# Kernel optimization log

Hardware: AMD Instinct MI355X
Metric: run time of the kernel (lower is better)

Reference implementation:

```python
import jax, jax.numpy as jnp
import numpy as np

B, T, C = 4, 8192, 1024
H, D = 16, 64  # n_head, head_dim


def setup_inputs() -> dict:
    key = jax.random.key(0)
    ks = jax.random.split(key, 9)
    s = 1.0 / np.sqrt(C)
    return {
        "x": jax.random.normal(ks[0], (B, T, C), jnp.float32),
        "Wq": jax.random.uniform(ks[1], (C, C), jnp.float32, -s, s),
        "bq": jax.random.uniform(ks[2], (C,), jnp.float32, -s, s),
        "Wk": jax.random.uniform(ks[3], (C, C), jnp.float32, -s, s),
        "bk": jax.random.uniform(ks[4], (C,), jnp.float32, -s, s),
        "Wv": jax.random.uniform(ks[5], (C, C), jnp.float32, -s, s),
        "bv": jax.random.uniform(ks[6], (C,), jnp.float32, -s, s),
        "Wp": jax.random.uniform(ks[7], (C, C), jnp.float32, -s, s),
        "bp": jax.random.uniform(ks[8], (C,), jnp.float32, -s, s),
    }


def _heads(t):
    # (B,T,C) -> (B,H,T,D)
    return t.reshape(B, T, H, D).transpose(0, 2, 1, 3)


def reference(x, Wq, bq, Wk, bk, Wv, bv, Wp, bp):
    q = _heads(x @ Wq.T + bq)
    k = _heads(x @ Wk.T + bk)
    v = _heads(x @ Wv.T + bv)
    # attn_type='l1': softmax q,k over feature dim; L1 normalizer
    q = jax.nn.softmax(q, axis=-1)
    k = jax.nn.softmax(k, axis=-1)
    k_sum = k.sum(axis=-2, keepdims=True)               # (B,H,1,D)
    D_inv = 1.0 / (q * k_sum).sum(axis=-1, keepdims=True)  # (B,H,T,1)
    context = jnp.einsum('bhtd,bhte->bhde', k, v)       # (B,H,D,D)
    out = jnp.einsum('bhtd,bhde->bhte', q, context) * D_inv + q
    out = out.transpose(0, 2, 1, 3).reshape(B, T, C)
    return out @ Wp.T + bp
```

## Files before the change

kernel.cpp:

```cpp
#include <hip/hip_runtime.h>
#include <hip/hip_bf16.h>
#include <stdint.h>


#define BT    32768
#define CDIM  1024

using bf16 = __hip_bfloat16;
typedef short  short8   __attribute__((ext_vector_type(8)));
typedef short  short4_t __attribute__((ext_vector_type(4)));
typedef unsigned short ushort4_t __attribute__((ext_vector_type(4)));
typedef float  floatx4  __attribute__((ext_vector_type(4)));

__device__ __forceinline__ float bfbits2f(unsigned short u) {
    union { unsigned int i; float f; } c; c.i = ((unsigned int)u) << 16; return c.f;
}

__device__ __forceinline__ void gld_lds16(const void* g, void* lds) {
    __builtin_amdgcn_global_load_lds(
        (const __attribute__((address_space(1))) uint32_t*)g,
        (__attribute__((address_space(3))) uint32_t*)lds,
        16, 0, 0);
}

__global__ void zero_kernel(float* __restrict__ p) {
    p[(size_t)blockIdx.x * 256 + threadIdx.x] = 0.0f;
}

__global__ void cvt_kernel(const float* __restrict__ x,
                           const float* __restrict__ Wq, const float* __restrict__ Wk,
                           const float* __restrict__ Wv, const float* __restrict__ Wp,
                           bf16* __restrict__ xb, bf16* __restrict__ Wb) {
    const int XF4 = (BT * CDIM) / 4;
    int i = blockIdx.x * 256 + threadIdx.x;
    const float* src; bf16* dst; int off;
    if (i < XF4) { src = x; dst = xb; off = i; }
    else {
        int i2 = i - XF4;
        int wi = i2 >> 18;
        off = i2 & 0x3FFFF;
        src = (wi == 0) ? Wq : (wi == 1) ? Wk : (wi == 2) ? Wv : Wp;
        dst = Wb + (size_t)wi * 1048576;
    }
    float4 f = ((const float4*)src)[off];
    union { bf16 h[4]; short4_t v; } u;
    u.h[0] = __float2bfloat16(f.x); u.h[1] = __float2bfloat16(f.y);
    u.h[2] = __float2bfloat16(f.z); u.h[3] = __float2bfloat16(f.w);
    *(short4_t*)(dst + (size_t)off * 4) = u.v;
}

__global__ __launch_bounds__(256)
void gemm_qkv(const bf16* __restrict__ A, const bf16* __restrict__ Bw,
              const float* __restrict__ bq, const float* __restrict__ bk,
              const float* __restrict__ bv,
              bf16* __restrict__ qb, bf16* __restrict__ kb, bf16* __restrict__ vb) {
    __shared__ bf16 sA[128 * 32];
    __shared__ bf16 sB[128 * 32];
    int tid = threadIdx.x, lane = tid & 63, wv = tid >> 6;
    int bn = blockIdx.x % 24;
    int bm = blockIdx.x / 24;
    const bf16* Ab = A  + (size_t)bm * 128 * CDIM;
    const bf16* Bb = Bw + (size_t)bn * 128 * CDIM;
    int srow = lane >> 2;
    int scol = ((lane & 3) ^ ((lane >> 3) & 3)) * 8;

    floatx4 acc[4][4] = {};
    int quad = lane >> 4, l15 = lane & 15;
    int m0 = (wv & 1) * 64, n0v = (wv >> 1) * 64;
    int rpos = (quad ^ ((l15 >> 1) & 3)) * 8;

    for (int kt = 0; kt < 32; ++kt) {
        int k0 = kt * 32;
        #pragma unroll
        for (int c = 0; c < 2; ++c) {
            int chunk = wv * 2 + c;
            gld_lds16(Ab + (size_t)(chunk * 16 + srow) * CDIM + k0 + scol, &sA[chunk * 512]);
            gld_lds16(Bb + (size_t)(chunk * 16 + srow) * CDIM + k0 + scol, &sB[chunk * 512]);
        }
        __syncthreads();
        short8 af[4], bfr[4];
        #pragma unroll
        for (int i = 0; i < 4; ++i) {
            af[i]  = *(const short8*)&sA[(m0  + i * 16 + l15) * 32 + rpos];
            bfr[i] = *(const short8*)&sB[(n0v + i * 16 + l15) * 32 + rpos];
        }
        #pragma unroll
        for (int i = 0; i < 4; ++i)
            #pragma unroll
            for (int j = 0; j < 4; ++j)
                acc[i][j] = __builtin_amdgcn_mfma_f32_16x16x32_bf16(af[i], bfr[j], acc[i][j], 0, 0, 0);
        __syncthreads();
    }

    int grow0 = bm * 128 + m0;
    int n_abs = bn * 128 + n0v;
    bf16* dst; const float* biasp; int ncol0; bool smax;
    if (n_abs < 1024)      { dst = qb; biasp = bq; ncol0 = n_abs;        smax = true;  }
    else if (n_abs < 2048) { dst = kb; biasp = bk; ncol0 = n_abs - 1024; smax = true;  }
    else                   { dst = vb; biasp = bv; ncol0 = n_abs - 2048; smax = false; }
    float bias4[4];
    #pragma unroll
    for (int j = 0; j < 4; ++j) bias4[j] = biasp[ncol0 + j * 16 + l15];

    #pragma unroll
    for (int i = 0; i < 4; ++i) {
        #pragma unroll
        for (int r = 0; r < 4; ++r) {
            float vals[4];
            #pragma unroll
            for (int j = 0; j < 4; ++j) vals[j] = acc[i][j][r] + bias4[j];
            if (smax) {
                float mx = fmaxf(fmaxf(vals[0], vals[1]), fmaxf(vals[2], vals[3]));
                #pragma unroll
                for (int d = 1; d < 16; d <<= 1) mx = fmaxf(mx, __shfl_xor(mx, d));
                float s = 0.f;
                #pragma unroll
                for (int j = 0; j < 4; ++j) { vals[j] = __expf(vals[j] - mx); s += vals[j]; }
                #pragma unroll
                for (int d = 1; d < 16; d <<= 1) s += __shfl_xor(s, d);
                float rinv = 1.0f / s;
                #pragma unroll
                for (int j = 0; j < 4; ++j) vals[j] *= rinv;
            }
            size_t row = (size_t)(grow0 + i * 16 + quad * 4 + r);
            #pragma unroll
            for (int j = 0; j < 4; ++j)
                dst[row * 1024 + ncol0 + j * 16 + l15] = __float2bfloat16(vals[j]);
        }
    }
}

__global__ __launch_bounds__(256)
void ctx_kernel(const bf16* __restrict__ kbuf, const bf16* __restrict__ vbuf,
                float* __restrict__ ctx, float* __restrict__ ksum) {
    int bid = blockIdx.x;
    int head = bid >> 4, chunk = bid & 15;
    int b = head >> 4, h = head & 15;
    size_t rowbase = (size_t)b * 8192 + (size_t)chunk * 512;
    int coff = h * 64;
    __shared__ bf16 ks[64 * 64];
    __shared__ bf16 vs[64 * 64];
    int tid = threadIdx.x;
    int lrow = tid >> 2, lpart = tid & 3;
    int di = tid >> 4, ei = tid & 15;

    float acc[16];
    #pragma unroll
    for (int i = 0; i < 16; ++i) acc[i] = 0.f;
    float ksv[4] = {0.f, 0.f, 0.f, 0.f};

    size_t gbase = (rowbase + lrow) * 1024 + coff + lpart * 16;
    short8 pk0 = *(const short8*)(kbuf + gbase);
    short8 pk1 = *(const short8*)(kbuf + gbase + 8);
    short8 pv0 = *(const short8*)(vbuf + gbase);
    short8 pv1 = *(const short8*)(vbuf + gbase + 8);

    for (int st = 0; st < 8; ++st) {
        __syncthreads();
        *(short8*)&ks[lrow * 64 + lpart * 16]     = pk0;
        *(short8*)&ks[lrow * 64 + lpart * 16 + 8] = pk1;
        *(short8*)&vs[lrow * 64 + lpart * 16]     = pv0;
        *(short8*)&vs[lrow * 64 + lpart * 16 + 8] = pv1;
        __syncthreads();
        if (st < 7) {
            size_t g = gbase + (size_t)(st + 1) * 64 * 1024;
            pk0 = *(const short8*)(kbuf + g);
            pk1 = *(const short8*)(kbuf + g + 8);
            pv0 = *(const short8*)(vbuf + g);
            pv1 = *(const short8*)(vbuf + g + 8);
        }
        for (int t = 0; t < 64; ++t) {
            ushort4_t ku = *(const ushort4_t*)&ks[t * 64 + di * 4];
            ushort4_t vu = *(const ushort4_t*)&vs[t * 64 + ei * 4];
            float kd[4], ve[4];
            #pragma unroll
            for (int i = 0; i < 4; ++i) { kd[i] = bfbits2f(ku[i]); ve[i] = bfbits2f(vu[i]); }
            #pragma unroll
            for (int i = 0; i < 4; ++i)
                #pragma unroll
                for (int j = 0; j < 4; ++j)
                    acc[i * 4 + j] = fmaf(kd[i], ve[j], acc[i * 4 + j]);
            #pragma unroll
            for (int j = 0; j < 4; ++j) ksv[j] += kd[j];
        }
    }
    float* cptr = ctx + (size_t)head * 4096;
    #pragma unroll
    for (int i = 0; i < 4; ++i)
        #pragma unroll
        for (int j = 0; j < 4; ++j)
            atomicAdd(&cptr[(di * 4 + i) * 64 + ei * 4 + j], acc[i * 4 + j]);
    if (ei == 0) {
        #pragma unroll
        for (int j = 0; j < 4; ++j) atomicAdd(&ksum[head * 64 + di * 4 + j], ksv[j]);
    }
}

#define QS 72
__global__ __launch_bounds__(256)
void attn_kernel(const bf16* __restrict__ qbuf, const float* __restrict__ ctx,
                 const float* __restrict__ ksum, bf16* __restrict__ ab) {
    int bid = blockIdx.x;
    int head = bid >> 7, tb = bid & 127;
    int b = head >> 4, h = head & 15;
    size_t row0 = (size_t)b * 8192 + (size_t)tb * 64;
    int coff = h * 64;
    __shared__ bf16 qs[64 * QS];
    __shared__ bf16 cts[64 * QS];
    __shared__ float ksums[64];
    __shared__ float dinv[64];
    int tid = threadIdx.x, lane = tid & 63, wv = tid >> 6;

    {
        int lrow = tid >> 2, lpart = tid & 3;
        size_t g = (row0 + lrow) * 1024 + coff + lpart * 16;
        short8 q0 = *(const short8*)(qbuf + g);
        short8 q1 = *(const short8*)(qbuf + g + 8);
        *(short8*)&qs[lrow * QS + lpart * 16]     = q0;
        *(short8*)&qs[lrow * QS + lpart * 16 + 8] = q1;
    }
    {
        const float* cp = ctx + (size_t)head * 4096;
        #pragma unroll
        for (int it = 0; it < 4; ++it) {
            int fi = it * 256 + tid;
            int d = fi >> 4, e0 = (fi & 15) * 4;
            float4 f = ((const float4*)cp)[fi];
            cts[(e0 + 0) * QS + d] = __float2bfloat16(f.x);
            cts[(e0 + 1) * QS + d] = __float2bfloat16(f.y);
            cts[(e0 + 2) * QS + d] = __float2bfloat16(f.z);
            cts[(e0 + 3) * QS + d] = __float2bfloat16(f.w);
        }
    }
    if (tid < 64) ksums[tid] = ksum[head * 64 + tid];
    __syncthreads();

    {
        int t = tid >> 2, dg = tid & 3;
        float p = 0.f;
        #pragma unroll
        for (int j = 0; j < 16; ++j)
            p = fmaf(__bfloat162float(qs[t * QS + dg * 16 + j]), ksums[dg * 16 + j], p);
        p += __shfl_xor(p, 1);
        p += __shfl_xor(p, 2);
        if (dg == 0) dinv[t] = 1.0f / p;
    }
    __syncthreads();

    int quad = lane >> 4, l15 = lane & 15;
    int trow0 = wv * 16;
    short8 aF0 = *(const short8*)&qs[(trow0 + l15) * QS + quad * 8];
    short8 aF1 = *(const short8*)&qs[(trow0 + l15) * QS + 32 + quad * 8];
    floatx4 acc[4] = {};
    #pragma unroll
    for (int ni = 0; ni < 4; ++ni) {
        short8 b0 = *(const short8*)&cts[(ni * 16 + l15) * QS + quad * 8];
        short8 b1 = *(const short8*)&cts[(ni * 16 + l15) * QS + 32 + quad * 8];
        acc[ni] = __builtin_amdgcn_mfma_f32_16x16x32_bf16(aF0, b0, acc[ni], 0, 0, 0);
        acc[ni] = __builtin_amdgcn_mfma_f32_16x16x32_bf16(aF1, b1, acc[ni], 0, 0, 0);
    }
    float dv[4];
    #pragma unroll
    for (int r = 0; r < 4; ++r) dv[r] = dinv[trow0 + quad * 4 + r];
    #pragma unroll
    for (int ni = 0; ni < 4; ++ni) {
        #pragma unroll
        for (int r = 0; r < 4; ++r) {
            int row = trow0 + quad * 4 + r;
            int col = ni * 16 + l15;
            float val = acc[ni][r] * dv[r] + __bfloat162float(qs[row * QS + col]);
            ab[(row0 + row) * 1024 + coff + col] = __float2bfloat16(val);
        }
    }
}

__global__ __launch_bounds__(256)
void gemm_out(const bf16* __restrict__ A, const bf16* __restrict__ Bw,
              const float* __restrict__ bp, float* __restrict__ outp) {
    __shared__ bf16 sA[128 * 32];
    __shared__ bf16 sB[128 * 32];
    int tid = threadIdx.x, lane = tid & 63, wv = tid >> 6;
    int bn = blockIdx.x & 7;
    int bm = blockIdx.x >> 3;
    const bf16* Ab = A  + (size_t)bm * 128 * CDIM;
    const bf16* Bb = Bw + (size_t)bn * 128 * CDIM;
    int srow = lane >> 2;
    int scol = ((lane & 3) ^ ((lane >> 3) & 3)) * 8;
    floatx4 acc[4][4] = {};
    int quad = lane >> 4, l15 = lane & 15;
    int m0 = (wv & 1) * 64, n0v = (wv >> 1) * 64;
    int rpos = (quad ^ ((l15 >> 1) & 3)) * 8;

    for (int kt = 0; kt < 32; ++kt) {
        int k0 = kt * 32;
        #pragma unroll
        for (int c = 0; c < 2; ++c) {
            int chunk = wv * 2 + c;
            gld_lds16(Ab + (size_t)(chunk * 16 + srow) * CDIM + k0 + scol, &sA[chunk * 512]);
            gld_lds16(Bb + (size_t)(chunk * 16 + srow) * CDIM + k0 + scol, &sB[chunk * 512]);
        }
        __syncthreads();
        short8 af[4], bfr[4];
        #pragma unroll
        for (int i = 0; i < 4; ++i) {
            af[i]  = *(const short8*)&sA[(m0  + i * 16 + l15) * 32 + rpos];
            bfr[i] = *(const short8*)&sB[(n0v + i * 16 + l15) * 32 + rpos];
        }
        #pragma unroll
        for (int i = 0; i < 4; ++i)
            #pragma unroll
            for (int j = 0; j < 4; ++j)
                acc[i][j] = __builtin_amdgcn_mfma_f32_16x16x32_bf16(af[i], bfr[j], acc[i][j], 0, 0, 0);
        __syncthreads();
    }
    int grow0 = bm * 128 + m0;
    int gcol0 = bn * 128 + n0v;
    float bias4[4];
    #pragma unroll
    for (int j = 0; j < 4; ++j) bias4[j] = bp[gcol0 + j * 16 + l15];
    #pragma unroll
    for (int i = 0; i < 4; ++i)
        #pragma unroll
        for (int r = 0; r < 4; ++r) {
            size_t row = (size_t)(grow0 + i * 16 + quad * 4 + r);
            #pragma unroll
            for (int j = 0; j < 4; ++j)
                outp[row * 1024 + gcol0 + j * 16 + l15] = acc[i][j][r] + bias4[j];
        }
}

extern "C" void kernel_launch(void* const* d_in, const int* in_sizes, int n_in,
                              void* d_out, int out_size, void* d_ws, size_t ws_size,
                              hipStream_t stream) {
    const float* x  = (const float*)d_in[0];
    const float* Wq = (const float*)d_in[1];
    const float* bq = (const float*)d_in[2];
    const float* Wk = (const float*)d_in[3];
    const float* bk = (const float*)d_in[4];
    const float* Wv = (const float*)d_in[5];
    const float* bv = (const float*)d_in[6];
    const float* Wp = (const float*)d_in[7];
    const float* bp = (const float*)d_in[8];
    float* outp = (float*)d_out;

    char* ws = (char*)d_ws;
    bf16*  xb   = (bf16*)(ws);
    bf16*  Wb   = (bf16*)(ws + 67108864);
    bf16*  qb   = (bf16*)(ws + 75497472);
    bf16*  kb   = (bf16*)(ws + 142606336);
    bf16*  vb   = (bf16*)(ws + 209715200);
    float* ctx  = (float*)(ws + 276824064);
    float* ksum = (float*)(ws + 277872640);
    bf16*  ab   = (bf16*)(ws);

    zero_kernel<<<1040, 256, 0, stream>>>(ctx);
    cvt_kernel<<<36864, 256, 0, stream>>>(x, Wq, Wk, Wv, Wp, xb, Wb);
    gemm_qkv<<<6144, 256, 0, stream>>>(xb, Wb, bq, bk, bv, qb, kb, vb);
    ctx_kernel<<<1024, 256, 0, stream>>>(kb, vb, ctx, ksum);
    attn_kernel<<<8192, 256, 0, stream>>>(qb, ctx, ksum, ab);
    gemm_out<<<2048, 256, 0, stream>>>(ab, Wb + (size_t)3072 * 1024, bp, outp);
}
```

Measured before the change: 726.2 us.

## Double GEMM K-tile to 64 with wider swizzle; pack ctx FMAs into float2

Both projection GEMMs now stage 64-wide K tiles per iteration instead of 32. That halves the number of barrier pairs and loop iterations, and the XOR swizzle is widened to 8 chunks to keep LDS reads conflict-free. The context kernel rewrites its rank-1 accumulation using float2 vectors, which can map to packed FP32 FMA instructions, and unrolls the time loop by 4. LDS use per GEMM block doubles, which may reduce occupancy.

```diff
diff --git a/kernel.cpp b/kernel.cpp
--- a/kernel.cpp
+++ b/kernel.cpp
@@ -11,6 +11,7 @@
 typedef short  short4_t __attribute__((ext_vector_type(4)));
 typedef unsigned short ushort4_t __attribute__((ext_vector_type(4)));
 typedef float  floatx4  __attribute__((ext_vector_type(4)));
+typedef float  float2v  __attribute__((ext_vector_type(2)));
 
 __device__ __forceinline__ float bfbits2f(unsigned short u) {
     union { unsigned int i; float f; } c; c.i = ((unsigned int)u) << 16; return c.f;
@@ -54,41 +55,45 @@
               const float* __restrict__ bq, const float* __restrict__ bk,
               const float* __restrict__ bv,
               bf16* __restrict__ qb, bf16* __restrict__ kb, bf16* __restrict__ vb) {
-    __shared__ bf16 sA[128 * 32];
-    __shared__ bf16 sB[128 * 32];
+    __shared__ bf16 sA[128 * 64];
+    __shared__ bf16 sB[128 * 64];
     int tid = threadIdx.x, lane = tid & 63, wv = tid >> 6;
     int bn = blockIdx.x % 24;
     int bm = blockIdx.x / 24;
     const bf16* Ab = A  + (size_t)bm * 128 * CDIM;
     const bf16* Bb = Bw + (size_t)bn * 128 * CDIM;
-    int srow = lane >> 2;
-    int scol = ((lane & 3) ^ ((lane >> 3) & 3)) * 8;
+    int srow8 = lane >> 3;
+    int scol = ((lane & 7) ^ ((lane >> 3) & 7)) * 8;
 
     floatx4 acc[4][4] = {};
     int quad = lane >> 4, l15 = lane & 15;
     int m0 = (wv & 1) * 64, n0v = (wv >> 1) * 64;
-    int rpos = (quad ^ ((l15 >> 1) & 3)) * 8;
-
-    for (int kt = 0; kt < 32; ++kt) {
-        int k0 = kt * 32;
-        #pragma unroll
-        for (int c = 0; c < 2; ++c) {
-            int chunk = wv * 2 + c;
-            gld_lds16(Ab + (size_t)(chunk * 16 + srow) * CDIM + k0 + scol, &sA[chunk * 512]);
-            gld_lds16(Bb + (size_t)(chunk * 16 + srow) * CDIM + k0 + scol, &sB[chunk * 512]);
-        }
-        __syncthreads();
-        short8 af[4], bfr[4];
-        #pragma unroll
-        for (int i = 0; i < 4; ++i) {
-            af[i]  = *(const short8*)&sA[(m0  + i * 16 + l15) * 32 + rpos];
-            bfr[i] = *(const short8*)&sB[(n0v + i * 16 + l15) * 32 + rpos];
-        }
-        #pragma unroll
-        for (int i = 0; i < 4; ++i)
-            #pragma unroll
-            for (int j = 0; j < 4; ++j)
-                acc[i][j] = __builtin_amdgcn_mfma_f32_16x16x32_bf16(af[i], bfr[j], acc[i][j], 0, 0, 0);
+
+    for (int kt = 0; kt < 16; ++kt) {
+        int k0 = kt * 64;
+        #pragma unroll
+        for (int c = 0; c < 4; ++c) {
+            int chunk = wv * 4 + c;
+            int row = chunk * 8 + srow8;
+            gld_lds16(Ab + (size_t)row * CDIM + k0 + scol, &sA[chunk * 512]);
+            gld_lds16(Bb + (size_t)row * CDIM + k0 + scol, &sB[chunk * 512]);
+        }
+        __syncthreads();
+        #pragma unroll
+        for (int sub = 0; sub < 2; ++sub) {
+            short8 af[4], bfr[4];
+            #pragma unroll
+            for (int i = 0; i < 4; ++i) {
+                int pa = ((sub * 4 + quad) ^ (l15 & 7)) * 8;
+                af[i]  = *(const short8*)&sA[(m0  + i * 16 + l15) * 64 + pa];
+                bfr[i] = *(const short8*)&sB[(n0v + i * 16 + l15) * 64 + pa];
+            }
+            #pragma unroll
+            for (int i = 0; i < 4; ++i)
+                #pragma unroll
+                for (int j = 0; j < 4; ++j)
+                    acc[i][j] = __builtin_amdgcn_mfma_f32_16x16x32_bf16(af[i], bfr[j], acc[i][j], 0, 0, 0);
+        }
         __syncthreads();
     }
 
@@ -144,10 +149,10 @@
     int lrow = tid >> 2, lpart = tid & 3;
     int di = tid >> 4, ei = tid & 15;
 
-    float acc[16];
-    #pragma unroll
-    for (int i = 0; i < 16; ++i) acc[i] = 0.f;
-    float ksv[4] = {0.f, 0.f, 0.f, 0.f};
+    float2v acc2[8];
+    #pragma unroll
+    for (int i = 0; i < 8; ++i) acc2[i] = (float2v){0.f, 0.f};
+    float2v ks2[2] = {(float2v){0.f, 0.f}, (float2v){0.f, 0.f}};
 
     size_t gbase = (rowbase + lrow) * 1024 + coff + lpart * 16;
     short8 pk0 = *(const short8*)(kbuf + gbase);
@@ -169,28 +174,36 @@
             pv0 = *(const short8*)(vbuf + g);
             pv1 = *(const short8*)(vbuf + g + 8);
         }
+        #pragma unroll 4
         for (int t = 0; t < 64; ++t) {
             ushort4_t ku = *(const ushort4_t*)&ks[t * 64 + di * 4];
             ushort4_t vu = *(const ushort4_t*)&vs[t * 64 + ei * 4];
-            float kd[4], ve[4];
-            #pragma unroll
-            for (int i = 0; i < 4; ++i) { kd[i] = bfbits2f(ku[i]); ve[i] = bfbits2f(vu[i]); }
-            #pragma unroll
-            for (int i = 0; i < 4; ++i)
-                #pragma unroll
-                for (int j = 0; j < 4; ++j)
-                    acc[i * 4 + j] = fmaf(kd[i], ve[j], acc[i * 4 + j]);
-            #pragma unroll
-            for (int j = 0; j < 4; ++j) ksv[j] += kd[j];
+            float kd[4];
+            #pragma unroll
+            for (int i = 0; i < 4; ++i) kd[i] = bfbits2f(ku[i]);
+            float2v vp0 = (float2v){bfbits2f(vu[0]), bfbits2f(vu[1])};
+            float2v vp1 = (float2v){bfbits2f(vu[2]), bfbits2f(vu[3])};
+            #pragma unroll
+            for (int i = 0; i < 4; ++i) {
+                float2v kb2 = (float2v){kd[i], kd[i]};
+                acc2[i * 2 + 0] += kb2 * vp0;
+                acc2[i * 2 + 1] += kb2 * vp1;
+            }
+            ks2[0] += (float2v){kd[0], kd[1]};
+            ks2[1] += (float2v){kd[2], kd[3]};
         }
     }
     float* cptr = ctx + (size_t)head * 4096;
     #pragma unroll
-    for (int i = 0; i < 4; ++i)
-        #pragma unroll
-        for (int j = 0; j < 4; ++j)
-            atomicAdd(&cptr[(di * 4 + i) * 64 + ei * 4 + j], acc[i * 4 + j]);
+    for (int i = 0; i < 4; ++i) {
+        #pragma unroll
+        for (int j = 0; j < 4; ++j) {
+            float v = (j & 1) ? acc2[i * 2 + (j >> 1)].y : acc2[i * 2 + (j >> 1)].x;
+            atomicAdd(&cptr[(di * 4 + i) * 64 + ei * 4 + j], v);
+        }
+    }
     if (ei == 0) {
+        float ksv[4] = {ks2[0].x, ks2[0].y, ks2[1].x, ks2[1].y};
         #pragma unroll
         for (int j = 0; j < 4; ++j) atomicAdd(&ksum[head * 64 + di * 4 + j], ksv[j]);
     }
@@ -277,40 +290,44 @@
 __global__ __launch_bounds__(256)
 void gemm_out(const bf16* __restrict__ A, const bf16* __restrict__ Bw,
               const float* __restrict__ bp, float* __restrict__ outp) {
-    __shared__ bf16 sA[128 * 32];
-    __shared__ bf16 sB[128 * 32];
+    __shared__ bf16 sA[128 * 64];
+    __shared__ bf16 sB[128 * 64];
     int tid = threadIdx.x, lane = tid & 63, wv = tid >> 6;
     int bn = blockIdx.x & 7;
     int bm = blockIdx.x >> 3;
     const bf16* Ab = A  + (size_t)bm * 128 * CDIM;
     const bf16* Bb = Bw + (size_t)bn * 128 * CDIM;
-    int srow = lane >> 2;
-    int scol = ((lane & 3) ^ ((lane >> 3) & 3)) * 8;
+    int srow8 = lane >> 3;
+    int scol = ((lane & 7) ^ ((lane >> 3) & 7)) * 8;
     floatx4 acc[4][4] = {};
     int quad = lane >> 4, l15 = lane & 15;
     int m0 = (wv & 1) * 64, n0v = (wv >> 1) * 64;
-    int rpos = (quad ^ ((l15 >> 1) & 3)) * 8;
-
-    for (int kt = 0; kt < 32; ++kt) {
-        int k0 = kt * 32;
-        #pragma unroll
-        for (int c = 0; c < 2; ++c) {
-            int chunk = wv * 2 + c;
-            gld_lds16(Ab + (size_t)(chunk * 16 + srow) * CDIM + k0 + scol, &sA[chunk * 512]);
-            gld_lds16(Bb + (size_t)(chunk * 16 + srow) * CDIM + k0 + scol, &sB[chunk * 512]);
-        }
-        __syncthreads();
-        short8 af[4], bfr[4];
-        #pragma unroll
-        for (int i = 0; i < 4; ++i) {
-            af[i]  = *(const short8*)&sA[(m0  + i * 16 + l15) * 32 + rpos];
-            bfr[i] = *(const short8*)&sB[(n0v + i * 16 + l15) * 32 + rpos];
-        }
-        #pragma unroll
-        for (int i = 0; i < 4; ++i)
-            #pragma unroll
-            for (int j = 0; j < 4; ++j)
-                acc[i][j] = __builtin_amdgcn_mfma_f32_16x16x32_bf16(af[i], bfr[j], acc[i][j], 0, 0, 0);
+
+    for (int kt = 0; kt < 16; ++kt) {
+        int k0 = kt * 64;
+        #pragma unroll
+        for (int c = 0; c < 4; ++c) {
+            int chunk = wv * 4 + c;
+            int row = chunk * 8 + srow8;
+            gld_lds16(Ab + (size_t)row * CDIM + k0 + scol, &sA[chunk * 512]);
+            gld_lds16(Bb + (size_t)row * CDIM + k0 + scol, &sB[chunk * 512]);
+        }
+        __syncthreads();
+        #pragma unroll
+        for (int sub = 0; sub < 2; ++sub) {
+            short8 af[4], bfr[4];
+            #pragma unroll
+            for (int i = 0; i < 4; ++i) {
+                int pa = ((sub * 4 + quad) ^ (l15 & 7)) * 8;
+                af[i]  = *(const short8*)&sA[(m0  + i * 16 + l15) * 64 + pa];
+                bfr[i] = *(const short8*)&sB[(n0v + i * 16 + l15) * 64 + pa];
+            }
+            #pragma unroll
+            for (int i = 0; i < 4; ++i)
+                #pragma unroll
+                for (int j = 0; j < 4; ++j)
+                    acc[i][j] = __builtin_amdgcn_mfma_f32_16x16x32_bf16(af[i], bfr[j], acc[i][j], 0, 0, 0);
+        }
         __syncthreads();
     }
     int grow0 = bm * 128 + m0;
```

Result: slower. 749.1 us (+3.2%).
